# Optimization experiments

Hardware: AMD Instinct MI355X
Metric: run time of the kernel (lower is better)

## Reference

```python
import jax, jax.numpy as jnp
import numpy as np

NUM_HEADS = 8
LN_EPS = 1e-3  # keras LayerNormalization default epsilon


def _layer_norm(z, gamma, beta):
    m = jnp.mean(z, axis=-1, keepdims=True)
    v = jnp.mean(jnp.square(z - m), axis=-1, keepdims=True)
    return (z - m) * jax.lax.rsqrt(v + LN_EPS) * gamma + beta


def _swish(z):
    return z * jax.nn.sigmoid(z)


def setup_inputs() -> dict:
    key = jax.random.key(0)
    ks = jax.random.split(key, 9)
    B, T, F, U = 64, 256, 512, 1024
    he = lambda k, s: jax.random.normal(k, s, jnp.float32) * np.sqrt(2.0 / s[0])
    glorot = lambda k, s: jax.random.normal(k, s, jnp.float32) * np.sqrt(2.0 / (s[0] + s[1]))
    return {
        "x": jax.random.normal(ks[0], (B, T, F), jnp.float32),
        "kernel_x": he(ks[1], (F, U)),
        "kernel_h": he(ks[2], (U, U)),
        "W_q": glorot(ks[3], (U, U)),
        "W_k": glorot(ks[4], (U, U)),
        "W_v": glorot(ks[5], (U, U)),
        "W_o": glorot(ks[6], (U, U)),
        "W_f": glorot(ks[7], (U, U)),
        "W_i": glorot(ks[8], (U, U)),
        "ln1_gamma": jnp.ones((U,), jnp.float32),
        "ln1_beta": jnp.zeros((U,), jnp.float32),
        "ln2_gamma": jnp.ones((U,), jnp.float32),
        "ln2_beta": jnp.zeros((U,), jnp.float32),
    }


def reference(x, kernel_x, kernel_h, W_q, W_k, W_v, W_o, W_f, W_i,
              ln1_gamma, ln1_beta, ln2_gamma, ln2_beta):
    B, T, F = x.shape
    U = kernel_x.shape[1]
    H = NUM_HEADS
    D = U // H
    scale = 1.0 / np.sqrt(D)

    def step(carry, x_t):
        h_prev, c_prev = carry  # c_prev = layer-normed longterm from last step
        xx = x_t @ kernel_x + h_prev @ kernel_h           # [B,U]
        f = jax.nn.sigmoid(xx @ W_f)
        i = jax.nn.sigmoid(xx @ W_i)
        cand = jnp.tanh(xx)
        longterm = f * c_prev + i * cand
        shortterm = _swish(longterm + _swish(xx))
        shortterm = _layer_norm(shortterm, ln1_gamma, ln1_beta)
        longterm = _layer_norm(longterm, ln2_gamma, ln2_beta)
        # mini self-attention where the "sequence" axis is the 8 heads
        q = (shortterm @ W_q).reshape(B, H, D)
        k = (shortterm @ W_k).reshape(B, H, D)
        v = (shortterm @ W_v).reshape(B, H, D)
        scores = jnp.einsum("bhd,bgd->bhg", q, k) * scale  # [B,H,H]
        weights = jax.nn.softmax(scores, axis=-1)
        attended = jnp.einsum("bhg,bgd->bhd", weights, v).reshape(B, U)
        out = shortterm + attended @ W_o
        return (out, longterm), out

    init = (jnp.zeros((B, U), x.dtype), jnp.zeros((B, U), x.dtype))
    _, ys = jax.lax.scan(step, init, jnp.swapaxes(x, 0, 1))  # ys: [T,B,U]
    return jnp.swapaxes(ys, 0, 1)  # [B,T,U]
```

## Files before the change

### kernel.cpp

```cpp
#include <hip/hip_runtime.h>

#define NB 64
#define NT 256
#define NF 512
#define NU 1024
#define NWG 256
#define NTHR 256
#define SLICE 65536

typedef float f32x4 __attribute__((ext_vector_type(4)));

__device__ __forceinline__ float sigm(float x) { return 1.f / (1.f + __expf(-x)); }

__device__ __forceinline__ f32x4 ld_cg4(const float* p) {
  f32x4 t;
  asm volatile("global_load_dwordx4 %0, %1, off sc0 sc1" : "=&v"(t) : "v"(p));
  return t;
}
__device__ __forceinline__ float ld_cg1(const float* p) {
  float t;
  asm volatile("global_load_dword %0, %1, off sc0 sc1" : "=&v"(t) : "v"(p));
  return t;
}
__device__ __forceinline__ f32x4 ld_nc4(const float* p) {
  f32x4 t;
  asm volatile("global_load_dwordx4 %0, %1, off" : "=&v"(t) : "v"(p));
  return t;
}
__device__ __forceinline__ void vm_wait() {
  asm volatile("s_waitcnt vmcnt(0)" ::: "memory");
  __builtin_amdgcn_sched_barrier(0);
}

struct KParams {
  const float *x, *g1, *b1, *g2, *b2;
  const float *Wx, *Wh, *Wf, *Wi, *Wq, *Wk, *Wv, *Wo;
  float *out;
  float *xxp, *fip, *qkvp, *wop;
  float *xxm, *lt, *sp, *c, *attb, *stats;
  int *flags, *grel;
};

__device__ __forceinline__ void grid_barrier(int* flags, int* grel, int epoch,
                                             int wg, int tid, bool dirty) {
  asm volatile("s_waitcnt vmcnt(0) lgkmcnt(0)" ::: "memory");
  __syncthreads();
  if (wg == 0) {
    if (tid > 0) {
      while (__hip_atomic_load(&flags[tid * 16], __ATOMIC_RELAXED, __HIP_MEMORY_SCOPE_AGENT) < epoch)
        __builtin_amdgcn_s_sleep(1);
    }
    __syncthreads();
    if (tid == 0)
      __builtin_amdgcn_fence(__ATOMIC_RELEASE, "agent");
    __syncthreads();
    if (tid < 16)
      __hip_atomic_store(&grel[tid * 16], epoch, __ATOMIC_RELAXED, __HIP_MEMORY_SCOPE_AGENT);
    __syncthreads();
  } else {
    if (tid == 0) {
      if (dirty)
        __builtin_amdgcn_fence(__ATOMIC_RELEASE, "agent");
      __hip_atomic_store(&flags[wg * 16], epoch, __ATOMIC_RELAXED, __HIP_MEMORY_SCOPE_AGENT);
      const int g = wg >> 4;
      while (__hip_atomic_load(&grel[g * 16], __ATOMIC_RELAXED, __HIP_MEMORY_SCOPE_AGENT) < epoch)
        __builtin_amdgcn_s_sleep(1);
    }
    __syncthreads();
  }
}

__device__ __forceinline__ void gemm_tile(
    float* As, float* Wl, const float* smm, const float* smr,
    int mode, const float* A0, size_t a_ld,
    const float* g1, const float* b1, const float* wop,
    float* outw, size_t out_ld,
    const float* __restrict__ W, int n0, int k0, int nchunks,
    float* __restrict__ dst, int tid)
{
  const int cg = tid & 15, rg = tid >> 4;
  const int c0 = cg * 4, r0 = rg * 4;
  float4 acc0 = {0,0,0,0}, acc1 = {0,0,0,0}, acc2 = {0,0,0,0}, acc3 = {0,0,0,0};

  for (int cc = 0; cc < nchunks; ++cc) {
    const int kc = k0 + cc * 64;
    __syncthreads();

    f32x4 wv[4];
#pragma unroll
    for (int it = 0; it < 4; ++it) {
      int idx = tid + it * 256;
      int kk = idx >> 4, cgs = idx & 15;
      wv[it] = ld_nc4(W + (size_t)(kc + kk) * NU + n0 + cgs * 4);
    }

    f32x4 v[4];
    if (mode == 0) {
#pragma unroll
      for (int it = 0; it < 4; ++it) {
        int idx = tid + it * 256;
        int r = idx >> 4, k4 = (idx & 15) << 2;
        v[it] = ld_nc4(A0 + (size_t)r * a_ld + kc + k4);
      }
    } else if (mode == 4) {
#pragma unroll
      for (int it = 0; it < 4; ++it) {
        int idx = tid + it * 256;
        int r = idx >> 4, k4 = (idx & 15) << 2;
        v[it] = ld_cg4(A0 + (size_t)r * a_ld + kc + k4);
      }
    } else if (mode == 3) {
      f32x4 av[4];
#pragma unroll
      for (int it = 0; it < 4; ++it) {
        int idx = tid + it * 256;
        int r = idx >> 4, k4 = (idx & 15) << 2;
        av[it] = ld_cg4(A0 + (size_t)r * NU + kc + k4);
      }
      vm_wait();
#pragma unroll
      for (int it = 0; it < 4; ++it) {
        int idx = tid + it * 256;
        int r = idx >> 4, k4 = (idx & 15) << 2;
        int col = kc + k4;
        float m = smm[r], rs = smr[r];
        f32x4 g  = *(const f32x4*)(g1 + col);
        f32x4 be = *(const f32x4*)(b1 + col);
        v[it] = (av[it] - m) * rs * g + be;
      }
    } else if (mode == 1) {
      if (A0) {
        f32x4 sv[4], w0v[4], w1v[4];
#pragma unroll
        for (int it = 0; it < 4; ++it) {
          int idx = tid + it * 256;
          int r = idx >> 4, k4 = (idx & 15) << 2;
          int col = kc + k4;
          sv[it]  = ld_cg4(A0 + (size_t)r * NU + col);
          w0v[it] = ld_cg4(wop + 0 * SLICE + (size_t)r * NU + col);
          w1v[it] = ld_cg4(wop + 1 * SLICE + (size_t)r * NU + col);
        }
        vm_wait();
        f32x4 pp[4];
#pragma unroll
        for (int it = 0; it < 4; ++it) {
          int idx = tid + it * 256;
          int r = idx >> 4, k4 = (idx & 15) << 2;
          int col = kc + k4;
          float m = smm[r], rs = smr[r];
          f32x4 g  = *(const f32x4*)(g1 + col);
          f32x4 be = *(const f32x4*)(b1 + col);
          pp[it] = (sv[it] - m) * rs * g + be + w0v[it] + w1v[it];
        }
#pragma unroll
        for (int it = 0; it < 4; ++it) {
          int idx = tid + it * 256;
          int r = idx >> 4, k4 = (idx & 15) << 2;
          int col = kc + k4;
          w0v[it] = ld_cg4(wop + 2 * SLICE + (size_t)r * NU + col);
          w1v[it] = ld_cg4(wop + 3 * SLICE + (size_t)r * NU + col);
        }
        vm_wait();
#pragma unroll
        for (int it = 0; it < 4; ++it) {
          int idx = tid + it * 256;
          int r = idx >> 4, k4 = (idx & 15) << 2;
          v[it] = pp[it] + w0v[it] + w1v[it];
          if (outw) *(f32x4*)(outw + (size_t)r * out_ld + kc + k4) = v[it];
        }
      } else {
#pragma unroll
        for (int it = 0; it < 4; ++it) v[it] = (f32x4){0.f, 0.f, 0.f, 0.f};
      }
    } else {
      f32x4 s0[4], s1[4], s2[4];
#pragma unroll
      for (int it = 0; it < 4; ++it) {
        int idx = tid + it * 256;
        int r = idx >> 4, k4 = (idx & 15) << 2;
        const float* bp = A0 + (size_t)r * NU + kc + k4;
        s0[it] = ld_cg4(bp);
        s1[it] = ld_cg4(bp + SLICE);
        s2[it] = ld_cg4(bp + 2 * SLICE);
      }
      vm_wait();
      f32x4 pp[4];
#pragma unroll
      for (int it = 0; it < 4; ++it) pp[it] = s0[it] + s1[it] + s2[it];
#pragma unroll
      for (int it = 0; it < 4; ++it) {
        int idx = tid + it * 256;
        int r = idx >> 4, k4 = (idx & 15) << 2;
        const float* bp = A0 + 3 * SLICE + (size_t)r * NU + kc + k4;
        s0[it] = ld_cg4(bp);
        s1[it] = ld_cg4(bp + SLICE);
        s2[it] = ld_cg4(bp + 2 * SLICE);
      }
      vm_wait();
#pragma unroll
      for (int it = 0; it < 4; ++it) {
        int idx = tid + it * 256;
        int r = idx >> 4, k4 = (idx & 15) << 2;
        v[it] = pp[it] + s0[it] + s1[it] + s2[it];
        if (outw) *(f32x4*)(outw + (size_t)r * NU + kc + k4) = v[it];
      }
    }

    vm_wait();
#pragma unroll
    for (int it = 0; it < 4; ++it) {
      int idx = tid + it * 256;
      int r = idx >> 4, k4 = (idx & 15) << 2;
      *(f32x4*)(&As[r * 68 + k4]) = v[it];
    }
#pragma unroll
    for (int it = 0; it < 4; ++it) {
      int idx = tid + it * 256;
      int kk = idx >> 4, cgs = idx & 15;
      int sw = (((kk >> 2) ^ cgs) & 15) << 2;
      int base = (cgs * 4) * 68 + sw + (kk & 3);
      Wl[base] = wv[it].x; Wl[base + 68] = wv[it].y; Wl[base + 136] = wv[it].z; Wl[base + 204] = wv[it].w;
    }
    __syncthreads();
#pragma unroll
    for (int kk = 0; kk < 64; kk += 4) {
      int sw = ((((kk >> 2) ^ cg) & 15) << 2);
      const float4 w0 = *(const float4*)(&Wl[(c0 + 0) * 68 + sw]);
      const float4 w1 = *(const float4*)(&Wl[(c0 + 1) * 68 + sw]);
      const float4 w2 = *(const float4*)(&Wl[(c0 + 2) * 68 + sw]);
      const float4 w3 = *(const float4*)(&Wl[(c0 + 3) * 68 + sw]);
      const float4 a0 = *(const float4*)(&As[(r0 + 0) * 68 + kk]);
      const float4 a1 = *(const float4*)(&As[(r0 + 1) * 68 + kk]);
      const float4 a2 = *(const float4*)(&As[(r0 + 2) * 68 + kk]);
      const float4 a3 = *(const float4*)(&As[(r0 + 3) * 68 + kk]);
#define DOT4(ac, av) \
      ac.x = fmaf(av.x, w0.x, fmaf(av.y, w0.y, fmaf(av.z, w0.z, fmaf(av.w, w0.w, ac.x)))); \
      ac.y = fmaf(av.x, w1.x, fmaf(av.y, w1.y, fmaf(av.z, w1.z, fmaf(av.w, w1.w, ac.y)))); \
      ac.z = fmaf(av.x, w2.x, fmaf(av.y, w2.y, fmaf(av.z, w2.z, fmaf(av.w, w2.w, ac.z)))); \
      ac.w = fmaf(av.x, w3.x, fmaf(av.y, w3.y, fmaf(av.z, w3.z, fmaf(av.w, w3.w, ac.w))));
      DOT4(acc0, a0) DOT4(acc1, a1) DOT4(acc2, a2) DOT4(acc3, a3)
#undef DOT4
    }
  }
  *(float4*)(dst + (size_t)(r0 + 0) * NU + n0 + c0) = acc0;
  *(float4*)(dst + (size_t)(r0 + 1) * NU + n0 + c0) = acc1;
  *(float4*)(dst + (size_t)(r0 + 2) * NU + n0 + c0) = acc2;
  *(float4*)(dst + (size_t)(r0 + 3) * NU + n0 + c0) = acc3;
}

__global__ __launch_bounds__(NTHR, 1) void vecaw_main(KParams p) {
  const int wg = blockIdx.x;
  const int tid = threadIdx.x;

  __shared__ __align__(16) float As[64 * 68];
  __shared__ __align__(16) float Wl[64 * 68];
  __shared__ float smm[64], smr[64], red[16], att_s[64];

  int epoch = 0;

  for (int t = 0; t < NT; ++t) {

    if (wg < 64) {
      const int nt = wg & 15, ks = wg >> 4;
      if (tid < 64 && t > 0) {
        float m = ld_cg1(p.stats + tid);
        float r = ld_cg1(p.stats + 64 + tid);
        vm_wait();
        smm[tid] = m; smr[tid] = r;
      }
      float* outw = (nt == 0 && t > 0) ? (p.out + (size_t)(t - 1) * NU) : nullptr;
      gemm_tile(As, Wl, smm, smr, 1, (t > 0) ? p.sp : nullptr, NU,
                p.g1, p.b1, p.wop, outw, (size_t)NT * NU,
                p.Wh, nt * 64, ks * 256, 4, p.xxp + (size_t)ks * SLICE, tid);
    } else if (wg < 96) {
      const int idx = wg - 64, nt = idx & 15, ks = idx >> 4;
      gemm_tile(As, Wl, nullptr, nullptr, 0, p.x + (size_t)t * NF, (size_t)NT * NF,
                nullptr, nullptr, nullptr, nullptr, 0,
                p.Wx, nt * 64, ks * 256, 4, p.xxp + (size_t)(4 + ks) * SLICE, tid);
    }
    grid_barrier(p.flags, p.grel, ++epoch, wg, tid, wg < 96);

    if (wg < 128) {
      const int mat = wg >> 6, idx = wg & 63, nt = idx & 15, ks = idx >> 4;
      float* outw = (mat == 0 && nt == 0) ? p.xxm : nullptr;
      gemm_tile(As, Wl, nullptr, nullptr, 2, p.xxp, NU,
                nullptr, nullptr, nullptr, outw, NU,
                mat ? p.Wi : p.Wf, nt * 64, ks * 256, 4,
                p.fip + (size_t)(mat * 4 + ks) * SLICE, tid);
    }
    grid_barrier(p.flags, p.grel, ++epoch, wg, tid, wg < 128);

    if (wg < 64) {
      const int b = wg;
      const size_t off = (size_t)b * NU + tid * 4;
      f32x4 xq = ld_cg4(p.xxm + off);
      f32x4 f0 = ld_cg4(p.fip + off);
      f32x4 f1 = ld_cg4(p.fip + SLICE + off);
      f32x4 f2 = ld_cg4(p.fip + 2 * SLICE + off);
      f32x4 f3 = ld_cg4(p.fip + 3 * SLICE + off);
      f32x4 i0 = ld_cg4(p.fip + 4 * SLICE + off);
      f32x4 i1 = ld_cg4(p.fip + 5 * SLICE + off);
      f32x4 i2 = ld_cg4(p.fip + 6 * SLICE + off);
      f32x4 i3 = ld_cg4(p.fip + 7 * SLICE + off);
      f32x4 cq = ld_cg4(p.c + off);
      vm_wait();
      f32x4 fsv = f0 + f1 + f2 + f3;
      f32x4 isv = i0 + i1 + i2 + i3;
      f32x4 ltq, spq;
#define P3COMP(C) { \
      float xxv = xq.C; \
      float f = sigm(fsv.C), i = sigm(isv.C); \
      float ltv = f * cq.C + i * tanhf(xxv); \
      float sw = xxv * sigm(xxv); \
      float spin = ltv + sw; \
      ltq.C = ltv; spq.C = spin * sigm(spin); }
      P3COMP(x) P3COMP(y) P3COMP(z) P3COMP(w)
#undef P3COMP
      *(f32x4*)(p.lt + off) = ltq;
      *(f32x4*)(p.sp + off) = spq;
      float s0 = spq.x + spq.y + spq.z + spq.w;
      float s1 = spq.x*spq.x + spq.y*spq.y + spq.z*spq.z + spq.w*spq.w;
      float s2 = ltq.x + ltq.y + ltq.z + ltq.w;
      float s3 = ltq.x*ltq.x + ltq.y*ltq.y + ltq.z*ltq.z + ltq.w*ltq.w;
#pragma unroll
      for (int m = 1; m < 64; m <<= 1) {
        s0 += __shfl_xor(s0, m, 64); s1 += __shfl_xor(s1, m, 64);
        s2 += __shfl_xor(s2, m, 64); s3 += __shfl_xor(s3, m, 64);
      }
      if ((tid & 63) == 0) {
        int wv = tid >> 6;
        red[wv * 4 + 0] = s0; red[wv * 4 + 1] = s1;
        red[wv * 4 + 2] = s2; red[wv * 4 + 3] = s3;
      }
      __syncthreads();
      if (tid == 0) {
        float S0 = red[0] + red[4] + red[8]  + red[12];
        float S1 = red[1] + red[5] + red[9]  + red[13];
        float S2 = red[2] + red[6] + red[10] + red[14];
        float S3 = red[3] + red[7] + red[11] + red[15];
        float m1 = S0 * (1.f / 1024.f), v1 = S1 * (1.f / 1024.f) - m1 * m1;
        float m2 = S2 * (1.f / 1024.f), v2 = S3 * (1.f / 1024.f) - m2 * m2;
        p.stats[b]       = m1;
        p.stats[64 + b]  = rsqrtf(v1 + 1e-3f);
        p.stats[128 + b] = m2;
        p.stats[192 + b] = rsqrtf(v2 + 1e-3f);
      }
    }
    grid_barrier(p.flags, p.grel, ++epoch, wg, tid, wg < 64);

    if (wg < 192) {
      if (tid < 64) {
        float m = ld_cg1(p.stats + tid);
        float r = ld_cg1(p.stats + 64 + tid);
        vm_wait();
        smm[tid] = m; smr[tid] = r;
      }
      const int mat = wg >> 6, idx = wg & 63, nt = idx & 15, ks = idx >> 4;
      const float* W = (mat == 0) ? p.Wq : (mat == 1) ? p.Wk : p.Wv;
      gemm_tile(As, Wl, smm, smr, 3, p.sp, NU,
                p.g1, p.b1, nullptr, nullptr, 0,
                W, nt * 64, ks * 256, 4, p.qkvp + (size_t)(mat * 4 + ks) * SLICE, tid);
    } else {
      const int b = wg - 192;
      float m  = ld_cg1(p.stats + 128 + b);
      float rv = ld_cg1(p.stats + 192 + b);
      f32x4 l4 = ld_cg4(p.lt + (size_t)b * NU + tid * 4);
      vm_wait();
      f32x4 g  = *(const f32x4*)(p.g2 + tid * 4);
      f32x4 be = *(const f32x4*)(p.b2 + tid * 4);
      f32x4 cv = (l4 - m) * rv * g + be;
      *(f32x4*)(p.c + (size_t)b * NU + tid * 4) = cv;
    }
    grid_barrier(p.flags, p.grel, ++epoch, wg, tid, true);

    if (wg < 64) {
      const int b = wg;
      f32x4 q0[3], q1[3], q2[3], q3[3];
#pragma unroll
      for (int it = 0; it < 3; ++it) {
        int e4 = (tid + it * 256) * 4;
        int m = e4 >> 10, d = e4 & 1023;
        const float* base = p.qkvp + (size_t)(m * 4) * SLICE + (size_t)b * NU + d;
        q0[it] = ld_cg4(base);
        q1[it] = ld_cg4(base + SLICE);
        q2[it] = ld_cg4(base + 2 * SLICE);
        q3[it] = ld_cg4(base + 3 * SLICE);
      }
      vm_wait();
#pragma unroll
      for (int it = 0; it < 3; ++it) {
        int e4 = (tid + it * 256) * 4;
        f32x4 s = q0[it] + q1[it] + q2[it] + q3[it];
        *(f32x4*)(&As[e4]) = s;
      }
      __syncthreads();
      if (tid < 64) {
        int h = tid >> 3, g = tid & 7;
        float s = 0.f;
#pragma unroll 8
        for (int d = 0; d < 128; ++d) s = fmaf(As[h * 128 + d], As[1024 + g * 128 + d], s);
        att_s[tid] = s * 0.08838834764831845f;
      }
      __syncthreads();
      if (tid < 8) {
        float mx = -1e30f;
#pragma unroll
        for (int g = 0; g < 8; ++g) mx = fmaxf(mx, att_s[tid * 8 + g]);
        float e8[8], sum = 0.f;
#pragma unroll
        for (int g = 0; g < 8; ++g) { e8[g] = __expf(att_s[tid * 8 + g] - mx); sum += e8[g]; }
        float inv = 1.f / sum;
#pragma unroll
        for (int g = 0; g < 8; ++g) att_s[tid * 8 + g] = e8[g] * inv;
      }
      __syncthreads();
      {
        int idx4 = tid * 4;
        int h = idx4 >> 7, d = idx4 & 127;
        f32x4 a = {0.f, 0.f, 0.f, 0.f};
#pragma unroll
        for (int g = 0; g < 8; ++g) {
          float w = att_s[h * 8 + g];
          a += w * (*(const f32x4*)(&As[2048 + g * 128 + d]));
        }
        *(f32x4*)(p.attb + (size_t)b * NU + idx4) = a;
      }
    }
    grid_barrier(p.flags, p.grel, ++epoch, wg, tid, wg < 64);

    if (wg < 64) {
      const int nt = wg & 15, ks = wg >> 4;
      gemm_tile(As, Wl, nullptr, nullptr, 4, p.attb, NU,
                nullptr, nullptr, nullptr, nullptr, 0,
                p.Wo, nt * 64, ks * 256, 4, p.wop + (size_t)ks * SLICE, tid);
    }
    grid_barrier(p.flags, p.grel, ++epoch, wg, tid, wg < 64);
  }

  if (wg < 64) {
    const int b = wg;
    const int u4 = tid * 4;
    const size_t off = (size_t)b * NU + u4;
    float m  = ld_cg1(p.stats + b);
    float rs = ld_cg1(p.stats + 64 + b);
    f32x4 s4 = ld_cg4(p.sp + off);
    f32x4 w0 = ld_cg4(p.wop + off);
    f32x4 w1 = ld_cg4(p.wop + SLICE + off);
    f32x4 w2 = ld_cg4(p.wop + 2 * SLICE + off);
    f32x4 w3 = ld_cg4(p.wop + 3 * SLICE + off);
    vm_wait();
    f32x4 g  = *(const f32x4*)(p.g1 + u4);
    f32x4 be = *(const f32x4*)(p.b1 + u4);
    f32x4 o = (s4 - m) * rs * g + be + w0 + w1 + w2 + w3;
    *(f32x4*)(p.out + ((size_t)b * NT + 255) * NU + u4) = o;
  }
}

extern "C" void kernel_launch(void* const* d_in, const int* in_sizes, int n_in,
                              void* d_out, int out_size, void* d_ws, size_t ws_size,
                              hipStream_t stream) {
  (void)in_sizes; (void)n_in; (void)out_size; (void)ws_size;
  const float* x  = (const float*)d_in[0];
  const float* Wx = (const float*)d_in[1];
  const float* Wh = (const float*)d_in[2];
  const float* Wq = (const float*)d_in[3];
  const float* Wk = (const float*)d_in[4];
  const float* Wv = (const float*)d_in[5];
  const float* Wo = (const float*)d_in[6];
  const float* Wf = (const float*)d_in[7];
  const float* Wi = (const float*)d_in[8];
  const float* g1 = (const float*)d_in[9];
  const float* b1 = (const float*)d_in[10];
  const float* g2 = (const float*)d_in[11];
  const float* b2 = (const float*)d_in[12];

  char* pp = (char*)d_ws;
  auto take = [&](size_t bytes) { char* r = pp; pp += (bytes + 255) & ~(size_t)255; return r; };
  int*   flags = (int*)take(256 * 16 * 4);
  int*   grel  = (int*)take(16 * 16 * 4);
  float* stats = (float*)take(2 * 256 * 4);
  float* c     = (float*)take((size_t)SLICE * 4);
  size_t zbytes = (size_t)(pp - (char*)d_ws);
  float* xxp   = (float*)take((size_t)6 * SLICE * 4);
  float* fip   = (float*)take((size_t)8 * SLICE * 4);
  float* qkvp  = (float*)take((size_t)12 * SLICE * 4);
  float* wop   = (float*)take((size_t)4 * SLICE * 4);
  float* xxm   = (float*)take((size_t)SLICE * 4);
  float* lt    = (float*)take((size_t)SLICE * 4);
  float* sp    = (float*)take((size_t)SLICE * 4);
  float* attb  = (float*)take((size_t)SLICE * 4);

  hipMemsetAsync(d_ws, 0, zbytes, stream);

  KParams kp;
  kp.x = x; kp.g1 = g1; kp.b1 = b1; kp.g2 = g2; kp.b2 = b2;
  kp.Wx = Wx; kp.Wh = Wh; kp.Wf = Wf; kp.Wi = Wi;
  kp.Wq = Wq; kp.Wk = Wk; kp.Wv = Wv; kp.Wo = Wo;
  kp.out = (float*)d_out;
  kp.xxp = xxp; kp.fip = fip; kp.qkvp = qkvp; kp.wop = wop;
  kp.xxm = xxm; kp.lt = lt; kp.sp = sp; kp.c = c; kp.attb = attb;
  kp.stats = stats; kp.flags = flags; kp.grel = grel;

  vecaw_main<<<dim3(NWG), dim3(NTHR), 0, stream>>>(kp);
}
```

Before: 22.56 ms.

## Precompose gate weights to drop dependent GEMM stage and a grid barrier

Precomputes Wh·Wf, Wh·Wi, Wx·Wf, Wx·Wi once at kernel start so the forget/input gate pre-activations are computed directly from h and x, in parallel with xx. This removes the serial xx→gate GEMM stage and its grid barrier at every timestep. The layer-normed longterm state is kept in registers, which drops the separate c-normalization pass and its buffers. The x-projection for the next step is also moved into the attention phase on otherwise idle workgroups. In exchange it adds a one-time large weight-product GEMM and more partial-sum traffic, and the changed summation order can shift numerics.

Result: faster. 21.65 ms (-4.1%).

```diff
diff --git a/kernel.cpp b/kernel.cpp
--- a/kernel.cpp
+++ b/kernel.cpp
@@ -36,8 +36,8 @@
   const float *x, *g1, *b1, *g2, *b2;
   const float *Wx, *Wh, *Wf, *Wi, *Wq, *Wk, *Wv, *Wo;
   float *out;
-  float *xxp, *fip, *qkvp, *wop;
-  float *xxm, *lt, *sp, *c, *attb, *stats;
+  float *xp, *qkvp, *wop, *attb, *sp, *stats;
+  float *WhWf, *WhWi, *WxWf, *WxWi;
   int *flags, *grel;
 };
 
@@ -128,7 +128,7 @@
         f32x4 be = *(const f32x4*)(b1 + col);
         v[it] = (av[it] - m) * rs * g + be;
       }
-    } else if (mode == 1) {
+    } else {
       if (A0) {
         f32x4 sv[4], w0v[4], w1v[4];
 #pragma unroll
@@ -171,38 +171,6 @@
       } else {
 #pragma unroll
         for (int it = 0; it < 4; ++it) v[it] = (f32x4){0.f, 0.f, 0.f, 0.f};
-      }
-    } else {
-      f32x4 s0[4], s1[4], s2[4];
-#pragma unroll
-      for (int it = 0; it < 4; ++it) {
-        int idx = tid + it * 256;
-        int r = idx >> 4, k4 = (idx & 15) << 2;
-        const float* bp = A0 + (size_t)r * NU + kc + k4;
-        s0[it] = ld_cg4(bp);
-        s1[it] = ld_cg4(bp + SLICE);
-        s2[it] = ld_cg4(bp + 2 * SLICE);
-      }
-      vm_wait();
-      f32x4 pp[4];
-#pragma unroll
-      for (int it = 0; it < 4; ++it) pp[it] = s0[it] + s1[it] + s2[it];
-#pragma unroll
-      for (int it = 0; it < 4; ++it) {
-        int idx = tid + it * 256;
-        int r = idx >> 4, k4 = (idx & 15) << 2;
-        const float* bp = A0 + 3 * SLICE + (size_t)r * NU + kc + k4;
-        s0[it] = ld_cg4(bp);
-        s1[it] = ld_cg4(bp + SLICE);
-        s2[it] = ld_cg4(bp + 2 * SLICE);
-      }
-      vm_wait();
-#pragma unroll
-      for (int it = 0; it < 4; ++it) {
-        int idx = tid + it * 256;
-        int r = idx >> 4, k4 = (idx & 15) << 2;
-        v[it] = pp[it] + s0[it] + s1[it] + s2[it];
-        if (outw) *(f32x4*)(outw + (size_t)r * NU + kc + k4) = v[it];
       }
     }
 
@@ -248,6 +216,17 @@
   *(float4*)(dst + (size_t)(r0 + 3) * NU + n0 + c0) = acc3;
 }
 
+__device__ __forceinline__ void run_xjob(const KParams& p, float* As, float* Wl,
+                                         int t, int j, int tid) {
+  const int out = j >> 5, rest = j & 31;
+  const int xs = rest >> 4, nt = rest & 15;
+  const float* W = (out == 0) ? p.Wx : (out == 1) ? p.WxWf : p.WxWi;
+  gemm_tile(As, Wl, nullptr, nullptr, 0, p.x + (size_t)t * NF, (size_t)NT * NF,
+            nullptr, nullptr, nullptr, nullptr, 0,
+            W, nt * 64, xs * 256, 4,
+            p.xp + (size_t)(out * 6 + 4 + xs) * SLICE, tid);
+}
+
 __global__ __launch_bounds__(NTHR, 1) void vecaw_main(KParams p) {
   const int wg = blockIdx.x;
   const int tid = threadIdx.x;
@@ -257,66 +236,63 @@
   __shared__ float smm[64], smr[64], red[16], att_s[64];
 
   int epoch = 0;
+  f32x4 c_reg = {0.f, 0.f, 0.f, 0.f};
+
+  for (int r = 0; r < 3; ++r) {
+    int j = r * 256 + wg;
+    const float *A0, *W; float *dst; int jj;
+    if (j < 256)      { jj = j;       A0 = p.Wh; W = p.Wf; dst = p.WhWf; }
+    else if (j < 512) { jj = j - 256; A0 = p.Wh; W = p.Wi; dst = p.WhWi; }
+    else if (j < 640) { jj = j - 512; A0 = p.Wx; W = p.Wf; dst = p.WxWf; }
+    else              { jj = j - 640; A0 = p.Wx; W = p.Wi; dst = p.WxWi; }
+    const int rb = jj >> 4, nt = jj & 15;
+    gemm_tile(As, Wl, nullptr, nullptr, 0, A0 + (size_t)rb * 64 * NU, NU,
+              nullptr, nullptr, nullptr, nullptr, 0,
+              W, nt * 64, 0, 16, dst + (size_t)rb * 64 * NU, tid);
+    grid_barrier(p.flags, p.grel, ++epoch, wg, tid, true);
+  }
+  if (wg < 96) run_xjob(p, As, Wl, 0, wg, tid);
+  grid_barrier(p.flags, p.grel, ++epoch, wg, tid, wg < 96);
 
   for (int t = 0; t < NT; ++t) {
 
-    if (wg < 64) {
-      const int nt = wg & 15, ks = wg >> 4;
+    if (wg < 192) {
+      const int out = wg >> 6, idx = wg & 63, nt = idx & 15, ks = idx >> 4;
       if (tid < 64 && t > 0) {
         float m = ld_cg1(p.stats + tid);
         float r = ld_cg1(p.stats + 64 + tid);
         vm_wait();
         smm[tid] = m; smr[tid] = r;
       }
-      float* outw = (nt == 0 && t > 0) ? (p.out + (size_t)(t - 1) * NU) : nullptr;
+      const float* W = (out == 0) ? p.Wh : (out == 1) ? p.WhWf : p.WhWi;
+      float* outw = (out == 0 && nt == 0 && t > 0) ? (p.out + (size_t)(t - 1) * NU) : nullptr;
       gemm_tile(As, Wl, smm, smr, 1, (t > 0) ? p.sp : nullptr, NU,
                 p.g1, p.b1, p.wop, outw, (size_t)NT * NU,
-                p.Wh, nt * 64, ks * 256, 4, p.xxp + (size_t)ks * SLICE, tid);
-    } else if (wg < 96) {
-      const int idx = wg - 64, nt = idx & 15, ks = idx >> 4;
-      gemm_tile(As, Wl, nullptr, nullptr, 0, p.x + (size_t)t * NF, (size_t)NT * NF,
-                nullptr, nullptr, nullptr, nullptr, 0,
-                p.Wx, nt * 64, ks * 256, 4, p.xxp + (size_t)(4 + ks) * SLICE, tid);
-    }
-    grid_barrier(p.flags, p.grel, ++epoch, wg, tid, wg < 96);
-
-    if (wg < 128) {
-      const int mat = wg >> 6, idx = wg & 63, nt = idx & 15, ks = idx >> 4;
-      float* outw = (mat == 0 && nt == 0) ? p.xxm : nullptr;
-      gemm_tile(As, Wl, nullptr, nullptr, 2, p.xxp, NU,
-                nullptr, nullptr, nullptr, outw, NU,
-                mat ? p.Wi : p.Wf, nt * 64, ks * 256, 4,
-                p.fip + (size_t)(mat * 4 + ks) * SLICE, tid);
-    }
-    grid_barrier(p.flags, p.grel, ++epoch, wg, tid, wg < 128);
+                W, nt * 64, ks * 256, 4,
+                p.xp + (size_t)(out * 6 + ks) * SLICE, tid);
+    }
+    grid_barrier(p.flags, p.grel, ++epoch, wg, tid, wg < 192);
 
     if (wg < 64) {
       const int b = wg;
       const size_t off = (size_t)b * NU + tid * 4;
-      f32x4 xq = ld_cg4(p.xxm + off);
-      f32x4 f0 = ld_cg4(p.fip + off);
-      f32x4 f1 = ld_cg4(p.fip + SLICE + off);
-      f32x4 f2 = ld_cg4(p.fip + 2 * SLICE + off);
-      f32x4 f3 = ld_cg4(p.fip + 3 * SLICE + off);
-      f32x4 i0 = ld_cg4(p.fip + 4 * SLICE + off);
-      f32x4 i1 = ld_cg4(p.fip + 5 * SLICE + off);
-      f32x4 i2 = ld_cg4(p.fip + 6 * SLICE + off);
-      f32x4 i3 = ld_cg4(p.fip + 7 * SLICE + off);
-      f32x4 cq = ld_cg4(p.c + off);
+      f32x4 a[18];
+#pragma unroll
+      for (int s = 0; s < 18; ++s) a[s] = ld_cg4(p.xp + (size_t)s * SLICE + off);
       vm_wait();
-      f32x4 fsv = f0 + f1 + f2 + f3;
-      f32x4 isv = i0 + i1 + i2 + i3;
+      f32x4 xx = a[0] + a[1] + a[2] + a[3] + a[4] + a[5];
+      f32x4 fs = a[6] + a[7] + a[8] + a[9] + a[10] + a[11];
+      f32x4 is = a[12] + a[13] + a[14] + a[15] + a[16] + a[17];
       f32x4 ltq, spq;
-#define P3COMP(C) { \
-      float xxv = xq.C; \
-      float f = sigm(fsv.C), i = sigm(isv.C); \
-      float ltv = f * cq.C + i * tanhf(xxv); \
+#define P2COMP(C) { \
+      float xxv = xx.C; \
+      float f = sigm(fs.C), i = sigm(is.C); \
+      float ltv = f * c_reg.C + i * tanhf(xxv); \
       float sw = xxv * sigm(xxv); \
       float spin = ltv + sw; \
       ltq.C = ltv; spq.C = spin * sigm(spin); }
-      P3COMP(x) P3COMP(y) P3COMP(z) P3COMP(w)
-#undef P3COMP
-      *(f32x4*)(p.lt + off) = ltq;
+      P2COMP(x) P2COMP(y) P2COMP(z) P2COMP(w)
+#undef P2COMP
       *(f32x4*)(p.sp + off) = spq;
       float s0 = spq.x + spq.y + spq.z + spq.w;
       float s1 = spq.x*spq.x + spq.y*spq.y + spq.z*spq.z + spq.w*spq.w;
@@ -333,17 +309,21 @@
         red[wv * 4 + 2] = s2; red[wv * 4 + 3] = s3;
       }
       __syncthreads();
-      if (tid == 0) {
+      {
         float S0 = red[0] + red[4] + red[8]  + red[12];
         float S1 = red[1] + red[5] + red[9]  + red[13];
         float S2 = red[2] + red[6] + red[10] + red[14];
         float S3 = red[3] + red[7] + red[11] + red[15];
         float m1 = S0 * (1.f / 1024.f), v1 = S1 * (1.f / 1024.f) - m1 * m1;
         float m2 = S2 * (1.f / 1024.f), v2 = S3 * (1.f / 1024.f) - m2 * m2;
-        p.stats[b]       = m1;
-        p.stats[64 + b]  = rsqrtf(v1 + 1e-3f);
-        p.stats[128 + b] = m2;
-        p.stats[192 + b] = rsqrtf(v2 + 1e-3f);
+        float rs2 = rsqrtf(v2 + 1e-3f);
+        f32x4 g2v = *(const f32x4*)(p.g2 + tid * 4);
+        f32x4 b2v = *(const f32x4*)(p.b2 + tid * 4);
+        c_reg = (ltq - m2) * rs2 * g2v + b2v;
+        if (tid == 0) {
+          p.stats[b]      = m1;
+          p.stats[64 + b] = rsqrtf(v1 + 1e-3f);
+        }
       }
     }
     grid_barrier(p.flags, p.grel, ++epoch, wg, tid, wg < 64);
@@ -360,18 +340,8 @@
       gemm_tile(As, Wl, smm, smr, 3, p.sp, NU,
                 p.g1, p.b1, nullptr, nullptr, 0,
                 W, nt * 64, ks * 256, 4, p.qkvp + (size_t)(mat * 4 + ks) * SLICE, tid);
-    } else {
-      const int b = wg - 192;
-      float m  = ld_cg1(p.stats + 128 + b);
-      float rv = ld_cg1(p.stats + 192 + b);
-      f32x4 l4 = ld_cg4(p.lt + (size_t)b * NU + tid * 4);
-      vm_wait();
-      f32x4 g  = *(const f32x4*)(p.g2 + tid * 4);
-      f32x4 be = *(const f32x4*)(p.b2 + tid * 4);
-      f32x4 cv = (l4 - m) * rv * g + be;
-      *(f32x4*)(p.c + (size_t)b * NU + tid * 4) = cv;
-    }
-    grid_barrier(p.flags, p.grel, ++epoch, wg, tid, true);
+    }
+    grid_barrier(p.flags, p.grel, ++epoch, wg, tid, wg < 192);
 
     if (wg < 64) {
       const int b = wg;
@@ -425,8 +395,10 @@
         }
         *(f32x4*)(p.attb + (size_t)b * NU + idx4) = a;
       }
-    }
-    grid_barrier(p.flags, p.grel, ++epoch, wg, tid, wg < 64);
+    } else if (wg < 160 && t + 1 < NT) {
+      run_xjob(p, As, Wl, t + 1, wg - 64, tid);
+    }
+    grid_barrier(p.flags, p.grel, ++epoch, wg, tid, wg < 160);
 
     if (wg < 64) {
       const int nt = wg & 15, ks = wg >> 4;
@@ -478,17 +450,17 @@
   auto take = [&](size_t bytes) { char* r = pp; pp += (bytes + 255) & ~(size_t)255; return r; };
   int*   flags = (int*)take(256 * 16 * 4);
   int*   grel  = (int*)take(16 * 16 * 4);
-  float* stats = (float*)take(2 * 256 * 4);
-  float* c     = (float*)take((size_t)SLICE * 4);
+  float* stats = (float*)take(256 * 4);
   size_t zbytes = (size_t)(pp - (char*)d_ws);
-  float* xxp   = (float*)take((size_t)6 * SLICE * 4);
-  float* fip   = (float*)take((size_t)8 * SLICE * 4);
+  float* xp    = (float*)take((size_t)18 * SLICE * 4);
   float* qkvp  = (float*)take((size_t)12 * SLICE * 4);
   float* wop   = (float*)take((size_t)4 * SLICE * 4);
-  float* xxm   = (float*)take((size_t)SLICE * 4);
-  float* lt    = (float*)take((size_t)SLICE * 4);
+  float* attb  = (float*)take((size_t)SLICE * 4);
   float* sp    = (float*)take((size_t)SLICE * 4);
-  float* attb  = (float*)take((size_t)SLICE * 4);
+  float* WhWf  = (float*)take((size_t)16 * SLICE * 4);
+  float* WhWi  = (float*)take((size_t)16 * SLICE * 4);
+  float* WxWf  = (float*)take((size_t)8 * SLICE * 4);
+  float* WxWi  = (float*)take((size_t)8 * SLICE * 4);
 
   hipMemsetAsync(d_ws, 0, zbytes, stream);
 
@@ -497,9 +469,10 @@
   kp.Wx = Wx; kp.Wh = Wh; kp.Wf = Wf; kp.Wi = Wi;
   kp.Wq = Wq; kp.Wk = Wk; kp.Wv = Wv; kp.Wo = Wo;
   kp.out = (float*)d_out;
-  kp.xxp = xxp; kp.fip = fip; kp.qkvp = qkvp; kp.wop = wop;
-  kp.xxm = xxm; kp.lt = lt; kp.sp = sp; kp.c = c; kp.attb = attb;
-  kp.stats = stats; kp.flags = flags; kp.grel = grel;
+  kp.xp = xp; kp.qkvp = qkvp; kp.wop = wop; kp.attb = attb; kp.sp = sp;
+  kp.stats = stats;
+  kp.WhWf = WhWf; kp.WhWi = WhWi; kp.WxWf = WxWf; kp.WxWi = WxWi;
+  kp.flags = flags; kp.grel = grel;
 
   vecaw_main<<<dim3(NWG), dim3(NTHR), 0, stream>>>(kp);
 }
```
